# Performance work log

Hardware: AMD Instinct MI355X
Metric: run time of the kernel (lower is better)

Reference implementation:

```python
import jax, jax.numpy as jnp
import numpy as np


def setup_inputs() -> dict:
    key = jax.random.key(0)
    k1, k2 = jax.random.split(key)
    N = 8192
    means = jax.random.normal(k1, (N, 3), dtype=jnp.float32) * 2.0
    normals = jax.random.normal(k2, (N, 3), dtype=jnp.float32)
    normals = normals / (jnp.linalg.norm(normals, axis=-1, keepdims=True) + 1e-8)
    return {"means": means, "normals": normals, "k": 8}


def reference(means, normals, k):
    # Pairwise Euclidean distances via the ||a-b||^2 expansion: avoids the
    # N x N x 3 diff tensor the original torch code materializes (same math).
    sq = jnp.sum(means * means, axis=-1)                      # (N,)
    d2 = sq[:, None] + sq[None, :] - 2.0 * (means @ means.T)  # (N, N)
    dists = jnp.sqrt(jnp.maximum(d2, 0.0))
    # k+1 smallest distances (self is the 0-distance nearest); drop self.
    dists = jax.lax.stop_gradient(dists)
    _, idx = jax.lax.top_k(-dists, k + 1)                     # (N, k+1)
    idx = idx[:, 1:]                                          # (N, k)
    neighbors = means[idx]                                    # (N, k, 3)
    local_diff = neighbors - means[:, None, :]                # (N, k, 3)
    plane_dist = jnp.sum(local_diff * normals[:, None, :], axis=-1)  # (N, k)
    return jnp.mean(jnp.abs(plane_dist))
```

## Files before the change

### kernel.cpp

```cpp
#include <hip/hip_runtime.h>
#include <hip/hip_bf16.h>

#define NPTS 8192
#define KNN 8
#define RPB 16
#define STAGES 8
#define SCOLS 1024

typedef __attribute__((ext_vector_type(8))) short bf16x8;
typedef __attribute__((ext_vector_type(4))) float f32x4;

__device__ __forceinline__ unsigned int bf16rne(float v) {
    unsigned int u = __float_as_uint(v);
    return (u + 0x7FFFu + ((u >> 16) & 1u)) >> 16;
}
__device__ __forceinline__ float bf2f(unsigned int h) { return __uint_as_float(h << 16); }

__device__ __forceinline__ void insert8(unsigned int (&best)[KNN], unsigned int key) {
#pragma unroll
    for (int t = 0; t < KNN; ++t) {
        const unsigned int lo = min(best[t], key);
        key = max(best[t], key);
        best[t] = lo;
    }
}
__device__ __forceinline__ void finsert8(float (&b)[KNN], float key) {
#pragma unroll
    for (int t = 0; t < KNN; ++t) {
        const float lo = fminf(b[t], key);
        key = fmaxf(b[t], key);
        b[t] = lo;
    }
}

__global__ __launch_bounds__(256) void pack_kernel(const float* __restrict__ means,
                                                   float4* __restrict__ pts,
                                                   uint4* __restrict__ cf0,
                                                   uint4* __restrict__ cf1,
                                                   uint4* __restrict__ rf0,
                                                   uint4* __restrict__ rf1,
                                                   float* __restrict__ out) {
    const int i = blockIdx.x * 256 + threadIdx.x;
    if (i == 0) out[0] = 0.0f;
    const float x = means[3 * i + 0];
    const float y = means[3 * i + 1];
    const float z = means[3 * i + 2];
    const float sq = x * x + y * y + z * z;
    pts[i] = make_float4(x, y, z, sq);
    const unsigned int hx = bf16rne(x), lx = bf16rne(x - bf2f(hx));
    const unsigned int hy = bf16rne(y), ly = bf16rne(y - bf2f(hy));
    const unsigned int hz = bf16rne(z), lz = bf16rne(z - bf2f(hz));
    const unsigned int hs = bf16rne(sq), ls = bf16rne(sq - bf2f(hs));
    cf0[i] = make_uint4(hx | (lx << 16), hx | (hy << 16),
                        ly | (hy << 16), hz | (lz << 16));
    cf1[i] = make_uint4(hz | (hs << 16), ls | (0x3F80u << 16), 0x3F80u, 0u);
    const float ax = -2.0f * x, ay = -2.0f * y, az = -2.0f * z;
    const unsigned int hax = bf16rne(ax), lax = bf16rne(ax - bf2f(hax));
    const unsigned int hay = bf16rne(ay), lay = bf16rne(ay - bf2f(hay));
    const unsigned int haz = bf16rne(az), laz = bf16rne(az - bf2f(haz));
    const unsigned int hsr = bf16rne(sq), lsr = bf16rne(sq - bf2f(hsr));
    rf0[i] = make_uint4(hax | (hax << 16), lax | (hay << 16),
                        hay | (lay << 16), haz | (haz << 16));
    rf1[i] = make_uint4(laz | (0x3F80u << 16), 0x3F80u | (hsr << 16), lsr, 0u);
}

__global__ __launch_bounds__(512) void mfma_knn(const uint4* __restrict__ cf0,
                                                const uint4* __restrict__ cf1,
                                                const uint4* __restrict__ rf0,
                                                const uint4* __restrict__ rf1,
                                                const float4* __restrict__ pts,
                                                const float* __restrict__ normals,
                                                float* __restrict__ out) {
    __shared__ unsigned int lds_acc[8][16][64];
    __shared__ float lds_min[16][33];
    __shared__ float lds_T[16];
    __shared__ unsigned int km[8][RPB][KNN + 1];
    const int tid = threadIdx.x;
    const int l = tid & 63;
    const int wv = __builtin_amdgcn_readfirstlane(tid >> 6);
    const int R = l & 15;
    const int g = l >> 4;
    const int arow = blockIdx.x * RPB + R;

    const float4 mp = pts[arow];

    uint4 bu = make_uint4(0u, 0u, 0u, 0u);
    if (g == 0) bu = rf0[arow];
    else if (g == 1) bu = rf1[arow];
    union { uint4 u; bf16x8 v; } Bf; Bf.u = bu;
    const f32x4 zero = {0.0f, 0.0f, 0.0f, 0.0f};

    const uint4* __restrict__ asel = (g == 1) ? cf1 : cf0;

    const int sp = (((int)blockIdx.x >> 6) + 1) & 7;
    {
        const int lbase = sp * SCOLS + wv * 128 + R;
        float lmin = 3.4e38f;
#pragma unroll
        for (int mt = 0; mt < 8; ++mt) {
            union { uint4 u; bf16x8 v; } Af;
            Af.u = asel[lbase + mt * 16];
            const f32x4 acc = __builtin_amdgcn_mfma_f32_16x16x32_bf16(Af.v, Bf.v, zero, 0, 0, 0);
            lmin = fminf(lmin, fminf(fminf(acc[0], acc[1]), fminf(acc[2], acc[3])));
        }
        lds_min[R][wv * 4 + g] = lmin;
    }
    __syncthreads();
    {
        const int row = wv * 2 + (l >> 5);
        float bb[KNN];
        bb[0] = lds_min[row][l & 31];
#pragma unroll
        for (int s = 1; s < KNN; ++s) bb[s] = 3.4e38f;
#pragma unroll
        for (int st = 1; st <= 16; st <<= 1) {
            float tk[KNN];
#pragma unroll
            for (int s = 0; s < KNN; ++s) tk[s] = __shfl_xor(bb[s], st);
#pragma unroll
            for (int s = 0; s < KNN; ++s) finsert8(bb, tk[s]);
        }
        if ((l & 31) == 0)
            lds_T[row] = bb[7] + 0.002f * fabsf(bb[7]) + 1e-5f;
    }
    __syncthreads();
    const float Tm = lds_T[R];

    unsigned int best[KNN];
#pragma unroll
    for (int s = 0; s < KNN; ++s) best[s] = ~0u;

#pragma unroll 1
    for (int s = 0; s < STAGES; ++s) {
        const int lbase = s * SCOLS + wv * 128 + R;
        const int cbase = s * SCOLS + wv * 128;
#pragma unroll
        for (int h = 0; h < 2; ++h) {
            unsigned int m = 0u;
#pragma unroll
            for (int mt4 = 0; mt4 < 4; ++mt4) {
                const int mt = h * 4 + mt4;
                union { uint4 u; bf16x8 v; } Af;
                Af.u = asel[lbase + mt * 16];
                const f32x4 acc = __builtin_amdgcn_mfma_f32_16x16x32_bf16(Af.v, Bf.v, zero, 0, 0, 0);
                lds_acc[wv][mt4 * 4 + 0][l] = __float_as_uint(acc[0]);
                lds_acc[wv][mt4 * 4 + 1][l] = __float_as_uint(acc[1]);
                lds_acc[wv][mt4 * 4 + 2][l] = __float_as_uint(acc[2]);
                lds_acc[wv][mt4 * 4 + 3][l] = __float_as_uint(acc[3]);
                m = m + m + ((acc[0] <= Tm) ? 1u : 0u);
                m = m + m + ((acc[1] <= Tm) ? 1u : 0u);
                m = m + m + ((acc[2] <= Tm) ? 1u : 0u);
                m = m + m + ((acc[3] <= Tm) ? 1u : 0u);
            }
            while (m) {
                const int b = __ffs(m) - 1;
                m &= m - 1;
                const int t = 15 - b;
                const float av = fmaxf(__uint_as_float(lds_acc[wv][t][l]), 0.0f);
                const int col = cbase + (h * 4 + (t >> 2)) * 16 + g * 4 + (t & 3);
                unsigned int key = (__float_as_uint(av) & 0xFFFFE000u) | (unsigned int)col;
                key = (col == arow) ? ~0u : key;
                insert8(best, key);
            }
        }
    }

#pragma unroll
    for (int st = 16; st <= 32; st <<= 1) {
        unsigned int tk[KNN];
#pragma unroll
        for (int s = 0; s < KNN; ++s) tk[s] = __shfl_xor(best[s], st);
#pragma unroll
        for (int s = 0; s < KNN; ++s) insert8(best, tk[s]);
    }
    if (l < RPB) {
#pragma unroll
        for (int s = 0; s < KNN; ++s) km[wv][l][s] = best[s];
    }
    for (int st = 1; st < 8; st <<= 1) {
        __syncthreads();
        if (((wv & (2 * st - 1)) == 0) && l < RPB) {
#pragma unroll
            for (int s = 0; s < KNN; ++s) insert8(best, km[wv + st][l][s]);
#pragma unroll
            for (int s = 0; s < KNN; ++s) km[wv][l][s] = best[s];
        }
    }

    if (wv == 0) {
        float sum = 0.0f;
        if (l < RPB) {
            const float nx = normals[3 * arow + 0];
            const float ny = normals[3 * arow + 1];
            const float nz = normals[3 * arow + 2];
#pragma unroll
            for (int s = 0; s < KNN; ++s) {
                const int nbr = (int)(best[s] & 0x1FFFu);
                const float4 q = pts[nbr];
                sum += fabsf((q.x - mp.x) * nx + (q.y - mp.y) * ny + (q.z - mp.z) * nz);
            }
        }
#pragma unroll
        for (int off = 8; off > 0; off >>= 1) sum += __shfl_down(sum, off);
        if (l == 0) atomicAdd(out, sum * (1.0f / ((float)NPTS * (float)KNN)));
    }
}

extern "C" void kernel_launch(void* const* d_in, const int* in_sizes, int n_in,
                              void* d_out, int out_size, void* d_ws, size_t ws_size,
                              hipStream_t stream) {
    const float* means = (const float*)d_in[0];
    const float* normals = (const float*)d_in[1];
    float* out = (float*)d_out;
    char* ws = (char*)d_ws;
    uint4* cf0 = (uint4*)ws;
    uint4* cf1 = (uint4*)(ws + 131072);
    uint4* rf0 = (uint4*)(ws + 262144);
    uint4* rf1 = (uint4*)(ws + 393216);
    float4* pts = (float4*)(ws + 524288);

    pack_kernel<<<NPTS / 256, 256, 0, stream>>>(means, pts, cf0, cf1, rf0, rf1, out);
    mfma_knn<<<NPTS / RPB, 512, 0, stream>>>(cf0, cf1, rf0, rf1, pts, normals, out);
}
```

Before: 38.73 us.

## Replace block-wide threshold prepass with per-lane running top-k threshold

Drops the sampling prepass that computed a shared per-row distance threshold through LDS, shuffle-based top-8 merges and two block barriers. Each lane now seeds its top-8 list directly from stage 0 and filters later stages against its own current 8th-best key, updated after each half-stage. This removes two __syncthreads and the float merge work. In exchange, each lane's threshold is looser at first because it has seen only its own columns, so more candidates may reach the serial insert loop and divergence may rise.

```diff
diff --git a/kernel.cpp b/kernel.cpp
--- a/kernel.cpp
+++ b/kernel.cpp
@@ -22,14 +22,6 @@
         const unsigned int lo = min(best[t], key);
         key = max(best[t], key);
         best[t] = lo;
-    }
-}
-__device__ __forceinline__ void finsert8(float (&b)[KNN], float key) {
-#pragma unroll
-    for (int t = 0; t < KNN; ++t) {
-        const float lo = fminf(b[t], key);
-        key = fmaxf(b[t], key);
-        b[t] = lo;
     }
 }
 
@@ -72,8 +64,6 @@
                                                 const float* __restrict__ normals,
                                                 float* __restrict__ out) {
     __shared__ unsigned int lds_acc[8][16][64];
-    __shared__ float lds_min[16][33];
-    __shared__ float lds_T[16];
     __shared__ unsigned int km[8][RPB][KNN + 1];
     const int tid = threadIdx.x;
     const int l = tid & 63;
@@ -92,46 +82,31 @@
 
     const uint4* __restrict__ asel = (g == 1) ? cf1 : cf0;
 
-    const int sp = (((int)blockIdx.x >> 6) + 1) & 7;
+    unsigned int best[KNN];
+#pragma unroll
+    for (int s = 0; s < KNN; ++s) best[s] = ~0u;
+
     {
-        const int lbase = sp * SCOLS + wv * 128 + R;
-        float lmin = 3.4e38f;
+        const int lbase = wv * 128 + R;
 #pragma unroll
         for (int mt = 0; mt < 8; ++mt) {
             union { uint4 u; bf16x8 v; } Af;
             Af.u = asel[lbase + mt * 16];
             const f32x4 acc = __builtin_amdgcn_mfma_f32_16x16x32_bf16(Af.v, Bf.v, zero, 0, 0, 0);
-            lmin = fminf(lmin, fminf(fminf(acc[0], acc[1]), fminf(acc[2], acc[3])));
-        }
-        lds_min[R][wv * 4 + g] = lmin;
-    }
-    __syncthreads();
-    {
-        const int row = wv * 2 + (l >> 5);
-        float bb[KNN];
-        bb[0] = lds_min[row][l & 31];
-#pragma unroll
-        for (int s = 1; s < KNN; ++s) bb[s] = 3.4e38f;
-#pragma unroll
-        for (int st = 1; st <= 16; st <<= 1) {
-            float tk[KNN];
-#pragma unroll
-            for (int s = 0; s < KNN; ++s) tk[s] = __shfl_xor(bb[s], st);
-#pragma unroll
-            for (int s = 0; s < KNN; ++s) finsert8(bb, tk[s]);
-        }
-        if ((l & 31) == 0)
-            lds_T[row] = bb[7] + 0.002f * fabsf(bb[7]) + 1e-5f;
-    }
-    __syncthreads();
-    const float Tm = lds_T[R];
-
-    unsigned int best[KNN];
-#pragma unroll
-    for (int s = 0; s < KNN; ++s) best[s] = ~0u;
+#pragma unroll
+            for (int r = 0; r < 4; ++r) {
+                const float av = fmaxf(acc[r], 0.0f);
+                const int col = wv * 128 + mt * 16 + g * 4 + r;
+                unsigned int key = (__float_as_uint(av) & 0xFFFFE000u) | (unsigned int)col;
+                key = (col == arow) ? ~0u : key;
+                insert8(best, key);
+            }
+        }
+    }
+    float bkT = __uint_as_float(best[7] | 0x1FFFu);
 
 #pragma unroll 1
-    for (int s = 0; s < STAGES; ++s) {
+    for (int s = 1; s < STAGES; ++s) {
         const int lbase = s * SCOLS + wv * 128 + R;
         const int cbase = s * SCOLS + wv * 128;
 #pragma unroll
@@ -147,10 +122,10 @@
                 lds_acc[wv][mt4 * 4 + 1][l] = __float_as_uint(acc[1]);
                 lds_acc[wv][mt4 * 4 + 2][l] = __float_as_uint(acc[2]);
                 lds_acc[wv][mt4 * 4 + 3][l] = __float_as_uint(acc[3]);
-                m = m + m + ((acc[0] <= Tm) ? 1u : 0u);
-                m = m + m + ((acc[1] <= Tm) ? 1u : 0u);
-                m = m + m + ((acc[2] <= Tm) ? 1u : 0u);
-                m = m + m + ((acc[3] <= Tm) ? 1u : 0u);
+                m = m + m + ((acc[0] <= bkT) ? 1u : 0u);
+                m = m + m + ((acc[1] <= bkT) ? 1u : 0u);
+                m = m + m + ((acc[2] <= bkT) ? 1u : 0u);
+                m = m + m + ((acc[3] <= bkT) ? 1u : 0u);
             }
             while (m) {
                 const int b = __ffs(m) - 1;
@@ -162,6 +137,7 @@
                 key = (col == arow) ? ~0u : key;
                 insert8(best, key);
             }
+            bkT = __uint_as_float(best[7] | 0x1FFFu);
         }
     }
 
```

Measured after the change: 46.39 us. 1.2x slower.
